# Optimization experiments

Hardware: AMD Instinct MI355X
Metric: run time of the kernel (lower is better)

## Reference

```python
import jax, jax.numpy as jnp
import numpy as np
import math

B, T, D, H = 4, 1024, 1024, 16
DK = D // H
TAU_THRESH = 0.3


def setup_inputs() -> dict:
    key = jax.random.key(0)
    ks = jax.random.split(key, 13)
    s = 1.0 / math.sqrt(D)
    return {
        "x": jax.random.normal(ks[0], (B, T, D), dtype=jnp.float32),
        "Wq": jax.random.normal(ks[1], (D, D), dtype=jnp.float32) * s,
        "bq": jax.random.normal(ks[2], (D,), dtype=jnp.float32) * s,
        "Wk": jax.random.normal(ks[3], (D, D), dtype=jnp.float32) * s,
        "bk": jax.random.normal(ks[4], (D,), dtype=jnp.float32) * s,
        "Wv": jax.random.normal(ks[5], (D, D), dtype=jnp.float32) * s,
        "bv": jax.random.normal(ks[6], (D,), dtype=jnp.float32) * s,
        "Wo": jax.random.normal(ks[7], (D, D), dtype=jnp.float32) * s,
        "bo": jax.random.normal(ks[8], (D,), dtype=jnp.float32) * s,
        "Wg1": jax.random.normal(ks[9], (1, D), dtype=jnp.float32) * s,
        "bg1": jax.random.normal(ks[10], (1,), dtype=jnp.float32) * s,
        "Wg2": jax.random.normal(ks[11], (1, D), dtype=jnp.float32) * s,
        "bg2": jax.random.normal(ks[12], (1,), dtype=jnp.float32) * s,
    }


def reference(x, Wq, bq, Wk, bk, Wv, bv, Wo, bo, Wg1, bg1, Wg2, bg2):
    b, t, d = x.shape
    # projections (torch Linear: y = x @ W.T + b)
    Q = (x @ Wq.T + bq).reshape(b, t, H, DK).transpose(0, 2, 1, 3)  # [B,H,T,dk]
    K = (x @ Wk.T + bk).reshape(b, t, H, DK).transpose(0, 2, 1, 3)
    V = (x @ Wv.T + bv).reshape(b, t, H, DK).transpose(0, 2, 1, 3)
    scores = jnp.einsum("bhqd,bhkd->bhqk", Q, K) / math.sqrt(DK)  # [B,H,T,T]
    # confidence gates from first-token query context [B, H*dk] = [B, D]
    context = Q[:, :, 0, :].reshape(b, d)
    q1 = jax.nn.sigmoid(context @ Wg1.T + bg1)  # [B,1]
    q2 = jax.nn.sigmoid(context @ Wg2.T + bg2)  # [B,1]
    c = jnp.clip(q1 * q2, 1e-8, 1.0)            # [B,1]
    tau = jnp.where(c < TAU_THRESH, 1.0 / c, jnp.ones_like(c)).reshape(b, 1, 1, 1)
    p = jax.nn.softmax(scores / tau, axis=-1)
    cb = c.reshape(b, 1, 1, 1)
    p_gated = cb * p + (1.0 - cb) * (1.0 / t)
    u = jnp.mean(1.0 - c, axis=-1, keepdims=True)  # [B,1]
    attn_out = jnp.einsum("bhqk,bhkd->bhqd", p_gated, V)
    attn_out = attn_out.transpose(0, 2, 1, 3).reshape(b, t, d)
    output = attn_out @ Wo.T + bo
    return output, u
```

## Files before the change

kernel.cpp:

```cpp
#include <hip/hip_runtime.h>
#include <stdint.h>

typedef short bf16x8 __attribute__((ext_vector_type(8)));
typedef float f32x4 __attribute__((ext_vector_type(4)));

#define MFMA_BF16(a, b, c) __builtin_amdgcn_mfma_f32_16x16x32_bf16((a), (b), (c), 0, 0, 0)

__device__ __forceinline__ short f2bf(float x) {
  union { float f; uint32_t u; } v; v.f = x;
  uint32_t r = (v.u + 0x7FFFu + ((v.u >> 16) & 1u)) >> 16;
  return (short)r;
}
__device__ __forceinline__ uint32_t rnd_bf_hi(float x) {
  union { float f; uint32_t u; } v; v.f = x;
  return v.u + 0x7FFFu + ((v.u >> 16) & 1u);
}
__device__ __forceinline__ uint32_t pack2bf(float a, float b) {
  return __builtin_amdgcn_perm(rnd_bf_hi(b), rnd_bf_hi(a), 0x07060302);
}
__device__ __forceinline__ float bfbits2f(uint32_t b16) {
  union { uint32_t u; float f; } v; v.u = b16 << 16; return v.f;
}
__device__ __forceinline__ float fexp2(float x) {
#if __has_builtin(__builtin_amdgcn_exp2f)
  return __builtin_amdgcn_exp2f(x);
#else
  return __expf(x * 0.6931471805599453f);
#endif
}
__device__ __forceinline__ void async16(const void* g, void* l) {
  __builtin_amdgcn_global_load_lds(
      (const __attribute__((address_space(1))) uint32_t*)g,
      (__attribute__((address_space(3))) uint32_t*)l, 16, 0, 0);
}

__global__ __launch_bounds__(256) void cvt_all(
    const float* __restrict__ x, const float* __restrict__ Wq,
    const float* __restrict__ Wk, const float* __restrict__ Wv,
    const float* __restrict__ Wo,
    short* __restrict__ xb, short* __restrict__ Wqb, short* __restrict__ Wkb,
    short* __restrict__ Wvb, short* __restrict__ Wob) {
  const int bid = blockIdx.x;
  const float* src; short* dst; int idx;
  if (bid < 4096) {
    src = x; dst = xb; idx = (bid << 8) + threadIdx.x;
  } else {
    const int r = bid - 4096;
    const int z = r >> 10;
    src = (z == 0) ? Wq : (z == 1) ? Wk : (z == 2) ? Wv : Wo;
    dst = (z == 0) ? Wqb : (z == 1) ? Wkb : (z == 2) ? Wvb : Wob;
    idx = ((r & 1023) << 8) + threadIdx.x;
  }
  float4 v = ((const float4*)src)[idx];
  short4 o;
  o.x = f2bf(v.x); o.y = f2bf(v.y); o.z = f2bf(v.z); o.w = f2bf(v.w);
  ((short4*)dst)[idx] = o;
}

__global__ __launch_bounds__(256) void gates_ctx(const float* __restrict__ x,
                                                 const float* __restrict__ Wq,
                                                 const float* __restrict__ bq,
                                                 float* __restrict__ ctx) {
  const int b = blockIdx.x;
  const int n0 = blockIdx.y << 6;
  __shared__ float xs[1024];
  const int tid = threadIdx.x;
  for (int i = tid; i < 1024; i += 256) xs[i] = x[b * 1048576 + i];
  __syncthreads();
  const int w = tid >> 6, lane = tid & 63;
  const float4* xv4 = (const float4*)xs;
  for (int rr = 0; rr < 16; ++rr) {
    const int n = n0 + (w << 4) + rr;
    const float4* wrow = (const float4*)(Wq + n * 1024);
    float p = 0.f;
#pragma unroll
    for (int c2 = 0; c2 < 4; ++c2) {
      float4 wv = wrow[lane + (c2 << 6)];
      float4 xv = xv4[lane + (c2 << 6)];
      p += xv.x * wv.x + xv.y * wv.y + xv.z * wv.z + xv.w * wv.w;
    }
#pragma unroll
    for (int off = 32; off; off >>= 1) p += __shfl_xor(p, off);
    if (lane == 0) ctx[b * 1024 + n] = p + bq[n];
  }
}

__global__ __launch_bounds__(256) void gates_fin(const float* __restrict__ ctx,
                                                 const float* __restrict__ Wg1,
                                                 const float* __restrict__ bg1,
                                                 const float* __restrict__ Wg2,
                                                 const float* __restrict__ bg2,
                                                 float* __restrict__ gates,
                                                 float* __restrict__ u_out) {
  __shared__ float red[16];
  const int tid = threadIdx.x, w = tid >> 6, lane = tid & 63;
  for (int b = 0; b < 4; ++b) {
    float4 cv = ((const float4*)(ctx + b * 1024))[tid];
    float4 w1 = ((const float4*)Wg1)[tid];
    float4 w2 = ((const float4*)Wg2)[tid];
    float p1 = cv.x * w1.x + cv.y * w1.y + cv.z * w1.z + cv.w * w1.w;
    float p2 = cv.x * w2.x + cv.y * w2.y + cv.z * w2.z + cv.w * w2.w;
#pragma unroll
    for (int off = 32; off; off >>= 1) { p1 += __shfl_xor(p1, off); p2 += __shfl_xor(p2, off); }
    if (lane == 0) { red[w] = p1; red[8 + w] = p2; }
    __syncthreads();
    if (tid == 0) {
      float g1 = red[0] + red[1] + red[2] + red[3] + bg1[0];
      float g2 = red[8] + red[9] + red[10] + red[11] + bg2[0];
      float q1 = 1.f / (1.f + expf(-g1));
      float q2 = 1.f / (1.f + expf(-g2));
      float c = fminf(fmaxf(q1 * q2, 1e-8f), 1.0f);
      gates[b * 2 + 0] = c;
      gates[b * 2 + 1] = (c < 0.3f ? c : 1.0f) * 0.125f;
      u_out[b] = 1.0f - c;
    }
    __syncthreads();
  }
}

__global__ __launch_bounds__(256) void gemm_qkv(
    const short* __restrict__ xb,
    const short* __restrict__ Wqb, const short* __restrict__ Wkb, const short* __restrict__ Wvb,
    const float* __restrict__ bq, const float* __restrict__ bk, const float* __restrict__ bv,
    const float* __restrict__ gat,
    short* __restrict__ Qh, short* __restrict__ Kh, short* __restrict__ Vt) {
  const int z = blockIdx.z;
  const short* W = (z == 0) ? Wqb : (z == 1) ? Wkb : Wvb;
  const float* bias = (z == 0) ? bq : (z == 1) ? bk : bv;

  const int m0 = blockIdx.x << 7;
  const int n0 = blockIdx.y << 7;
  const int tid = threadIdx.x;
  const int w = tid >> 6, lane = tid & 63;
  const int m15 = lane & 15, quad = lane >> 4;
  const int wr = w >> 1, wc = w & 1;

  const float qsc = (z == 0) ? gat[(m0 >> 10) * 2 + 1] * 1.4426950408889634f : 1.0f;

  __shared__ short As[4096];
  __shared__ short Bs[4096];
  __shared__ short Ts2[8192];

  f32x4 acc[4][4];
#pragma unroll
  for (int i = 0; i < 4; ++i)
#pragma unroll
    for (int j = 0; j < 4; ++j) { f32x4 zz = {0.f, 0.f, 0.f, 0.f}; acc[i][j] = zz; }

  const int srow = (w << 5) + (lane >> 2);
  const int scol = (lane & 3) << 3;
  const short* ga0 = xb + (m0 + srow) * 1024 + scol;
  const short* ga1 = ga0 + 16 * 1024;
  const short* gb0 = W + (n0 + srow) * 1024 + scol;
  const short* gb1 = gb0 + 16 * 1024;
  short* la0 = &As[srow * 32 + scol];
  short* la1 = la0 + 512;
  short* lb0 = &Bs[srow * 32 + scol];
  short* lb1 = lb0 + 512;

  for (int kt = 0; kt < 32; ++kt) {
    async16(ga0, la0); async16(ga1, la1);
    async16(gb0, lb0); async16(gb1, lb1);
    ga0 += 32; ga1 += 32; gb0 += 32; gb1 += 32;
    __syncthreads();
    bf16x8 a[4], b[4];
#pragma unroll
    for (int i = 0; i < 4; ++i)
      a[i] = *(const bf16x8*)(&As[((wr << 6) + (i << 4) + m15) * 32 + (quad << 3)]);
#pragma unroll
    for (int j = 0; j < 4; ++j)
      b[j] = *(const bf16x8*)(&Bs[((wc << 6) + (j << 4) + m15) * 32 + (quad << 3)]);
#pragma unroll
    for (int i = 0; i < 4; ++i)
#pragma unroll
      for (int j = 0; j < 4; ++j)
        acc[i][j] = MFMA_BF16(a[i], b[j], acc[i][j]);
    __syncthreads();
  }

  if (z == 2) {
    short* Ts = (w == 0) ? &As[0] : (w == 1) ? &Bs[0] : &Ts2[(w - 2) << 12];
    const int batch = m0 >> 10;
    const int tb0 = (m0 & 1023) + (wr << 6);
    const int h = (n0 >> 6) + wc;
#pragma unroll
    for (int j = 0; j < 4; ++j) {
      const int dkl = (j << 4) + m15;
      const float bb_ = bias[n0 + (wc << 6) + dkl];
#pragma unroll
      for (int i = 0; i < 4; ++i) {
        uint2 pk;
        pk.x = pack2bf(acc[i][j][0] + bb_, acc[i][j][1] + bb_);
        pk.y = pack2bf(acc[i][j][2] + bb_, acc[i][j][3] + bb_);
        const int blk = (i << 1) + (quad >> 1);
        const int addr = (dkl << 6) + ((blk ^ (dkl & 7)) << 3) + ((quad & 1) << 2);
        *(uint2*)&Ts[addr] = pk;
      }
    }
    __syncthreads();
    const int tb = lane & 7, dr = lane >> 3;
#pragma unroll
    for (int it = 0; it < 8; ++it) {
      const int dkl = dr + (it << 3);
      const int addr = (dkl << 6) + ((tb ^ (dkl & 7)) << 3);
      uint4 vv = *(const uint4*)&Ts[addr];
      *(uint4*)(Vt + ((((batch << 4) + h) << 6) + dkl) * 1024 + tb0 + (tb << 3)) = vv;
    }
  } else {
#pragma unroll
    for (int j = 0; j < 4; ++j) {
      const int n = n0 + (wc << 6) + (j << 4) + m15;
      const float bb_ = bias[n];
      const int h = n >> 6, dk = n & 63;
#pragma unroll
      for (int i = 0; i < 4; ++i) {
        const int mb = m0 + (wr << 6) + (i << 4) + (quad << 2);
#pragma unroll
        for (int r = 0; r < 4; ++r) {
          const int m = mb + r;
          const int batch = m >> 10, t = m & 1023;
          const short o = f2bf((acc[i][j][r] + bb_) * qsc);
          if (z == 1) Kh[((batch * 16 + h) * 1024 + t) * 64 + dk] = o;
          else        Qh[((batch * 16 + h) * 1024 + t) * 64 + dk] = o;
        }
      }
    }
  }
}

__global__ __launch_bounds__(256) void gemm_out(const short* __restrict__ Ab,
                                                const short* __restrict__ Wo,
                                                const float* __restrict__ bo,
                                                float* __restrict__ Cout) {
  const int m0 = blockIdx.x << 6;
  const int n0 = blockIdx.y << 7;
  const int tid = threadIdx.x;
  const int w = tid >> 6, lane = tid & 63;
  const int m15 = lane & 15, quad = lane >> 4;
  const int wr = w >> 1, wc = w & 1;

  __shared__ short As[2048];
  __shared__ short Bs[4096];

  f32x4 acc[2][4];
#pragma unroll
  for (int i = 0; i < 2; ++i)
#pragma unroll
    for (int j = 0; j < 4; ++j) { f32x4 zz = {0.f, 0.f, 0.f, 0.f}; acc[i][j] = zz; }

  const int arow = tid >> 2;
  const int acol = (tid & 3) << 3;
  const short* gA = Ab + (m0 + arow) * 1024 + acol;
  short* lA = &As[arow * 32 + acol];

  const int srow = (w << 5) + (lane >> 2);
  const int scol = (lane & 3) << 3;
  const short* gB0 = Wo + (n0 + srow) * 1024 + scol;
  const short* gB1 = gB0 + 16 * 1024;
  short* lB0 = &Bs[srow * 32 + scol];
  short* lB1 = lB0 + 512;

  for (int kt = 0; kt < 32; ++kt) {
    async16(gA, lA);
    async16(gB0, lB0); async16(gB1, lB1);
    gA += 32; gB0 += 32; gB1 += 32;
    __syncthreads();
    bf16x8 a[2], b[4];
#pragma unroll
    for (int i = 0; i < 2; ++i)
      a[i] = *(const bf16x8*)(&As[((wr << 5) + (i << 4) + m15) * 32 + (quad << 3)]);
#pragma unroll
    for (int j = 0; j < 4; ++j)
      b[j] = *(const bf16x8*)(&Bs[((wc << 6) + (j << 4) + m15) * 32 + (quad << 3)]);
#pragma unroll
    for (int i = 0; i < 2; ++i)
#pragma unroll
      for (int j = 0; j < 4; ++j)
        acc[i][j] = MFMA_BF16(a[i], b[j], acc[i][j]);
    __syncthreads();
  }

#pragma unroll
  for (int j = 0; j < 4; ++j) {
    const int n = n0 + (wc << 6) + (j << 4) + m15;
    const float bb_ = bo[n];
#pragma unroll
    for (int i = 0; i < 2; ++i) {
      const int mb = m0 + (wr << 5) + (i << 4) + (quad << 2);
#pragma unroll
      for (int r = 0; r < 4; ++r)
        Cout[(mb + r) * 1024 + n] = acc[i][j][r] + bb_;
    }
  }
}

__global__ __launch_bounds__(256) void meanv_k(const short* __restrict__ Vt,
                                               float* __restrict__ meanV) {
  const int bh = blockIdx.x;
  const int tid = threadIdx.x;
  const int d = tid >> 2, part = tid & 3;
  const short* row = Vt + bh * 65536 + d * 1024 + part * 256;
  float s = 0.f;
#pragma unroll 4
  for (int i = 0; i < 64; ++i) {
    uint2 v = *(const uint2*)(row + i * 4);
    s += bfbits2f(v.x & 0xffffu) + bfbits2f(v.x >> 16) +
         bfbits2f(v.y & 0xffffu) + bfbits2f(v.y >> 16);
  }
  s += __shfl_xor(s, 1);
  s += __shfl_xor(s, 2);
  if (part == 0) meanV[bh * 64 + d] = s * (1.0f / 1024.0f);
}

__global__ __launch_bounds__(256, 4) void attn_k(const short* __restrict__ Qh,
                                                 const short* __restrict__ Kh,
                                                 const short* __restrict__ Vt,
                                                 const float* __restrict__ gates,
                                                 const float* __restrict__ meanV,
                                                 short* __restrict__ attnb) {
  const int bh = blockIdx.x;
  const int b = bh >> 4, h = bh & 15;
  const int q0 = blockIdx.y << 6;
  const int tid = threadIdx.x;
  const int w = tid >> 6, lane = tid & 63;
  const int m15 = lane & 15, quad = lane >> 4;

  __shared__ short Ks[2][4096];
  __shared__ short Vs[2][4096];

  const short* ksrc = Kh + bh * 65536;
  const short* vsrc = Vt + bh * 65536;

  const short* qsrc = Qh + ((bh << 10) + q0 + (w << 4) + m15) * 64;
  const bf16x8 qb0 = *(const bf16x8*)(qsrc + (quad << 3));
  const bf16x8 qb1 = *(const bf16x8*)(qsrc + 32 + (quad << 3));

  const int off0 = tid, off1 = tid + 256;
  const int r0 = off0 >> 3, cb0 = (off0 & 7) ^ (r0 & 7);
  const int r1 = off1 >> 3, cb1 = (off1 & 7) ^ (r1 & 7);

#define STAGE(kv, bufi)                                                        \
  do {                                                                         \
    async16(ksrc + (((kv) << 6) + r0) * 64 + (cb0 << 3), &Ks[bufi][off0 << 3]);\
    async16(ksrc + (((kv) << 6) + r1) * 64 + (cb1 << 3), &Ks[bufi][off1 << 3]);\
    async16(vsrc + r0 * 1024 + ((kv) << 6) + (cb0 << 3), &Vs[bufi][off0 << 3]);\
    async16(vsrc + r1 * 1024 + ((kv) << 6) + (cb1 << 3), &Vs[bufi][off1 << 3]);\
  } while (0)

  STAGE(0, 0);

  float lsum = 0.f;
  f32x4 o_acc[4];
#pragma unroll
  for (int jd = 0; jd < 4; ++jd) { f32x4 zz = {0.f, 0.f, 0.f, 0.f}; o_acc[jd] = zz; }

  const int srcA = ((quad & 1) << 5) + m15;
  const int srcB = srcA + 16;
  const bool selhi = (quad & 2) != 0;

  for (int kv = 0; kv < 16; ++kv) {
    __syncthreads();
    if (kv < 15) STAGE(kv + 1, (kv + 1) & 1);
    const short* Kb = &Ks[kv & 1][0];
    const short* Vb = &Vs[kv & 1][0];

    f32x4 sacc[4];
#pragma unroll
    for (int s = 0; s < 4; ++s) {
      const int row = (s << 4) + m15;
      const int sw = row & 7;
      bf16x8 a0 = *(const bf16x8*)(Kb + (row << 6) + ((quad ^ sw) << 3));
      bf16x8 a1 = *(const bf16x8*)(Kb + (row << 6) + (((quad + 4) ^ sw) << 3));
      f32x4 zz = {0.f, 0.f, 0.f, 0.f};
      zz = MFMA_BF16(a0, qb0, zz);
      zz = MFMA_BF16(a1, qb1, zz);
      sacc[s] = zz;
    }

    uint32_t pk[4][2];
#pragma unroll
    for (int s = 0; s < 4; ++s) {
      float p0 = fexp2(sacc[s][0]);
      float p1 = fexp2(sacc[s][1]);
      float p2 = fexp2(sacc[s][2]);
      float p3 = fexp2(sacc[s][3]);
      lsum += (p0 + p1) + (p2 + p3);
      pk[s][0] = pack2bf(p0, p1);
      pk[s][1] = pack2bf(p2, p3);
    }

    bf16x8 pf[2];
#pragma unroll
    for (int H = 0; H < 2; ++H) {
      uint32_t f[4];
#pragma unroll
      for (int rp = 0; rp < 2; ++rp) {
        uint32_t alo = (uint32_t)__shfl((int)pk[2 * H][rp], srcA);
        uint32_t ahi = (uint32_t)__shfl((int)pk[2 * H + 1][rp], srcA);
        uint32_t blo = (uint32_t)__shfl((int)pk[2 * H][rp], srcB);
        uint32_t bhi = (uint32_t)__shfl((int)pk[2 * H + 1][rp], srcB);
        f[rp]     = selhi ? ahi : alo;
        f[2 + rp] = selhi ? bhi : blo;
      }
      pf[H] = *(bf16x8*)f;
    }

#pragma unroll
    for (int jd = 0; jd < 4; ++jd) {
      const int row = (jd << 4) + m15;
      const int sw = row & 7;
      bf16x8 v0 = *(const bf16x8*)(Vb + (row << 6) + ((quad ^ sw) << 3));
      bf16x8 v1 = *(const bf16x8*)(Vb + (row << 6) + (((quad + 4) ^ sw) << 3));
      o_acc[jd] = MFMA_BF16(v0, pf[0], o_acc[jd]);
      o_acc[jd] = MFMA_BF16(v1, pf[1], o_acc[jd]);
    }
  }
#undef STAGE

  float l = lsum;
  l += __shfl_xor(l, 16);
  l += __shfl_xor(l, 32);

  const float cg = gates[b * 2 + 0];
  const float s0 = cg / l;
  const float omc = 1.0f - cg;
  const int qrow = q0 + (w << 4) + m15;
  short* orow = attnb + ((b << 10) + qrow) * 1024 + (h << 6);
#pragma unroll
  for (int jd = 0; jd < 4; ++jd) {
    float4 mv = *(const float4*)(meanV + (bh << 6) + (jd << 4) + (quad << 2));
    float v0_ = s0 * o_acc[jd][0] + omc * mv.x;
    float v1_ = s0 * o_acc[jd][1] + omc * mv.y;
    float v2_ = s0 * o_acc[jd][2] + omc * mv.z;
    float v3_ = s0 * o_acc[jd][3] + omc * mv.w;
    uint2 st;
    st.x = pack2bf(v0_, v1_);
    st.y = pack2bf(v2_, v3_);
    *(uint2*)(orow + (jd << 4) + (quad << 2)) = st;
  }
}

extern "C" void kernel_launch(void* const* d_in, const int* in_sizes, int n_in,
                              void* d_out, int out_size, void* d_ws, size_t ws_size,
                              hipStream_t stream) {
  const float* x   = (const float*)d_in[0];
  const float* Wq  = (const float*)d_in[1];
  const float* bq  = (const float*)d_in[2];
  const float* Wk  = (const float*)d_in[3];
  const float* bk  = (const float*)d_in[4];
  const float* Wv  = (const float*)d_in[5];
  const float* bv  = (const float*)d_in[6];
  const float* Wo  = (const float*)d_in[7];
  const float* bo  = (const float*)d_in[8];
  const float* Wg1 = (const float*)d_in[9];
  const float* bg1 = (const float*)d_in[10];
  const float* Wg2 = (const float*)d_in[11];
  const float* bg2 = (const float*)d_in[12];
  float* out = (float*)d_out;

  char* ws = (char*)d_ws;
  short* xb   = (short*)(ws + 0);
  short* Wqb  = (short*)(ws + 8388608);
  short* Wkb  = (short*)(ws + 10485760);
  short* Wvb  = (short*)(ws + 12582912);
  short* Wob  = (short*)(ws + 14680064);
  short* Qh   = (short*)(ws + 16777216);
  short* Kh   = (short*)(ws + 25165824);
  short* Vt   = (short*)(ws + 33554432);
  short* attb = (short*)(ws + 41943040);
  float* ctx  = (float*)(ws + 50331648);
  float* gat  = (float*)(ws + 50348032);
  float* mV   = (float*)(ws + 50348064);

  cvt_all<<<8192, 256, 0, stream>>>(x, Wq, Wk, Wv, Wo, xb, Wqb, Wkb, Wvb, Wob);

  gates_ctx<<<dim3(4, 16), 256, 0, stream>>>(x, Wq, bq, ctx);
  gates_fin<<<1, 256, 0, stream>>>(ctx, Wg1, bg1, Wg2, bg2, gat, out + 4194304);

  gemm_qkv<<<dim3(32, 8, 3), 256, 0, stream>>>(xb, Wqb, Wkb, Wvb, bq, bk, bv, gat, Qh, Kh, Vt);
  meanv_k<<<64, 256, 0, stream>>>(Vt, mV);
  attn_k<<<dim3(64, 16), 256, 0, stream>>>(Qh, Kh, Vt, gat, mV, attb);
  gemm_out<<<dim3(64, 8), 256, 0, stream>>>(attb, Wob, bo, out);
}
```

Measured before the change: 222.3 us.

## Swizzle GEMM LDS tiles, fuse gate-context into conversion kernel, drop V transpose staging

Merges the fp32-to-bf16 conversion and gate-context matvec into one launch, removing a kernel launch. Both GEMMs now load LDS tiles with an XOR swizzle on the 16-byte column block, aimed at avoiding bank conflicts on the MFMA operand reads. The V projection epilogue no longer stages through shared memory for the transpose. It writes 8-byte packed chunks straight to the transposed Vt layout, which saves LDS space and a barrier but makes the global stores narrower and less coalesced.

```diff
diff --git a/kernel.cpp b/kernel.cpp
--- a/kernel.cpp
+++ b/kernel.cpp
@@ -34,54 +34,52 @@
       (__attribute__((address_space(3))) uint32_t*)l, 16, 0, 0);
 }
 
-__global__ __launch_bounds__(256) void cvt_all(
+__global__ __launch_bounds__(256) void prep_k(
     const float* __restrict__ x, const float* __restrict__ Wq,
     const float* __restrict__ Wk, const float* __restrict__ Wv,
-    const float* __restrict__ Wo,
+    const float* __restrict__ Wo, const float* __restrict__ bq,
     short* __restrict__ xb, short* __restrict__ Wqb, short* __restrict__ Wkb,
-    short* __restrict__ Wvb, short* __restrict__ Wob) {
+    short* __restrict__ Wvb, short* __restrict__ Wob, float* __restrict__ ctx) {
+  __shared__ float xs[1024];
   const int bid = blockIdx.x;
-  const float* src; short* dst; int idx;
-  if (bid < 4096) {
-    src = x; dst = xb; idx = (bid << 8) + threadIdx.x;
+  const int tid = threadIdx.x;
+  if (bid < 8192) {
+    const float* src; short* dst; int idx;
+    if (bid < 4096) {
+      src = x; dst = xb; idx = (bid << 8) + tid;
+    } else {
+      const int r = bid - 4096;
+      const int z = r >> 10;
+      src = (z == 0) ? Wq : (z == 1) ? Wk : (z == 2) ? Wv : Wo;
+      dst = (z == 0) ? Wqb : (z == 1) ? Wkb : (z == 2) ? Wvb : Wob;
+      idx = ((r & 1023) << 8) + tid;
+    }
+    float4 v = ((const float4*)src)[idx];
+    short4 o;
+    o.x = f2bf(v.x); o.y = f2bf(v.y); o.z = f2bf(v.z); o.w = f2bf(v.w);
+    ((short4*)dst)[idx] = o;
   } else {
-    const int r = bid - 4096;
-    const int z = r >> 10;
-    src = (z == 0) ? Wq : (z == 1) ? Wk : (z == 2) ? Wv : Wo;
-    dst = (z == 0) ? Wqb : (z == 1) ? Wkb : (z == 2) ? Wvb : Wob;
-    idx = ((r & 1023) << 8) + threadIdx.x;
-  }
-  float4 v = ((const float4*)src)[idx];
-  short4 o;
-  o.x = f2bf(v.x); o.y = f2bf(v.y); o.z = f2bf(v.z); o.w = f2bf(v.w);
-  ((short4*)dst)[idx] = o;
-}
-
-__global__ __launch_bounds__(256) void gates_ctx(const float* __restrict__ x,
-                                                 const float* __restrict__ Wq,
-                                                 const float* __restrict__ bq,
-                                                 float* __restrict__ ctx) {
-  const int b = blockIdx.x;
-  const int n0 = blockIdx.y << 6;
-  __shared__ float xs[1024];
-  const int tid = threadIdx.x;
-  for (int i = tid; i < 1024; i += 256) xs[i] = x[b * 1048576 + i];
-  __syncthreads();
-  const int w = tid >> 6, lane = tid & 63;
-  const float4* xv4 = (const float4*)xs;
-  for (int rr = 0; rr < 16; ++rr) {
-    const int n = n0 + (w << 4) + rr;
-    const float4* wrow = (const float4*)(Wq + n * 1024);
-    float p = 0.f;
-#pragma unroll
-    for (int c2 = 0; c2 < 4; ++c2) {
-      float4 wv = wrow[lane + (c2 << 6)];
-      float4 xv = xv4[lane + (c2 << 6)];
-      p += xv.x * wv.x + xv.y * wv.y + xv.z * wv.z + xv.w * wv.w;
-    }
-#pragma unroll
-    for (int off = 32; off; off >>= 1) p += __shfl_xor(p, off);
-    if (lane == 0) ctx[b * 1024 + n] = p + bq[n];
+    const int r = bid - 8192;
+    const int b = r >> 4;
+    const int n0 = (r & 15) << 6;
+    for (int i = tid; i < 1024; i += 256) xs[i] = x[b * 1048576 + i];
+    __syncthreads();
+    const int w = tid >> 6, lane = tid & 63;
+    const float4* xv4 = (const float4*)xs;
+    for (int rr = 0; rr < 16; ++rr) {
+      const int n = n0 + (w << 4) + rr;
+      const float4* wrow = (const float4*)(Wq + n * 1024);
+      float p = 0.f;
+#pragma unroll
+      for (int c2 = 0; c2 < 4; ++c2) {
+        float4 wv = wrow[lane + (c2 << 6)];
+        float4 xv = xv4[lane + (c2 << 6)];
+        p += xv.x * wv.x + xv.y * wv.y + xv.z * wv.z + xv.w * wv.w;
+      }
+#pragma unroll
+      for (int off = 32; off; off >>= 1) p += __shfl_xor(p, off);
+      if (lane == 0) ctx[b * 1024 + n] = p + bq[n];
+    }
   }
 }
 
@@ -139,7 +137,6 @@
 
   __shared__ short As[4096];
   __shared__ short Bs[4096];
-  __shared__ short Ts2[8192];
 
   f32x4 acc[4][4];
 #pragma unroll
@@ -147,16 +144,17 @@
 #pragma unroll
     for (int j = 0; j < 4; ++j) { f32x4 zz = {0.f, 0.f, 0.f, 0.f}; acc[i][j] = zz; }
 
-  const int srow = (w << 5) + (lane >> 2);
-  const int scol = (lane & 3) << 3;
-  const short* ga0 = xb + (m0 + srow) * 1024 + scol;
-  const short* ga1 = ga0 + 16 * 1024;
-  const short* gb0 = W + (n0 + srow) * 1024 + scol;
-  const short* gb1 = gb0 + 16 * 1024;
-  short* la0 = &As[srow * 32 + scol];
-  short* la1 = la0 + 512;
-  short* lb0 = &Bs[srow * 32 + scol];
-  short* lb1 = lb0 + 512;
+  const int s0 = tid, s1 = tid + 256;
+  const int row0 = s0 >> 2, lcb0 = (s0 & 3) ^ ((row0 >> 1) & 3);
+  const int row1 = s1 >> 2, lcb1 = (s1 & 3) ^ ((row1 >> 1) & 3);
+  const short* ga0 = xb + (m0 + row0) * 1024 + (lcb0 << 3);
+  const short* ga1 = xb + (m0 + row1) * 1024 + (lcb1 << 3);
+  const short* gb0 = W + (n0 + row0) * 1024 + (lcb0 << 3);
+  const short* gb1 = W + (n0 + row1) * 1024 + (lcb1 << 3);
+  short* la0 = &As[s0 << 3];
+  short* la1 = &As[s1 << 3];
+  short* lb0 = &Bs[s0 << 3];
+  short* lb1 = &Bs[s1 << 3];
 
   for (int kt = 0; kt < 32; ++kt) {
     async16(ga0, la0); async16(ga1, la1);
@@ -165,11 +163,15 @@
     __syncthreads();
     bf16x8 a[4], b[4];
 #pragma unroll
-    for (int i = 0; i < 4; ++i)
-      a[i] = *(const bf16x8*)(&As[((wr << 6) + (i << 4) + m15) * 32 + (quad << 3)]);
-#pragma unroll
-    for (int j = 0; j < 4; ++j)
-      b[j] = *(const bf16x8*)(&Bs[((wc << 6) + (j << 4) + m15) * 32 + (quad << 3)]);
+    for (int i = 0; i < 4; ++i) {
+      const int ra = (wr << 6) + (i << 4) + m15;
+      a[i] = *(const bf16x8*)(&As[ra * 32 + ((quad ^ ((ra >> 1) & 3)) << 3)]);
+    }
+#pragma unroll
+    for (int j = 0; j < 4; ++j) {
+      const int rb = (wc << 6) + (j << 4) + m15;
+      b[j] = *(const bf16x8*)(&Bs[rb * 32 + ((quad ^ ((rb >> 1) & 3)) << 3)]);
+    }
 #pragma unroll
     for (int i = 0; i < 4; ++i)
 #pragma unroll
@@ -179,32 +181,21 @@
   }
 
   if (z == 2) {
-    short* Ts = (w == 0) ? &As[0] : (w == 1) ? &Bs[0] : &Ts2[(w - 2) << 12];
     const int batch = m0 >> 10;
-    const int tb0 = (m0 & 1023) + (wr << 6);
-    const int h = (n0 >> 6) + wc;
 #pragma unroll
     for (int j = 0; j < 4; ++j) {
-      const int dkl = (j << 4) + m15;
-      const float bb_ = bias[n0 + (wc << 6) + dkl];
+      const int n = n0 + (wc << 6) + (j << 4) + m15;
+      const float bb_ = bias[n];
+      const int h = n >> 6, dk = n & 63;
+      short* vrow = Vt + ((((batch << 4) + h) << 6) + dk) * 1024;
 #pragma unroll
       for (int i = 0; i < 4; ++i) {
+        const int t = (m0 & 1023) + (wr << 6) + (i << 4) + (quad << 2);
         uint2 pk;
         pk.x = pack2bf(acc[i][j][0] + bb_, acc[i][j][1] + bb_);
         pk.y = pack2bf(acc[i][j][2] + bb_, acc[i][j][3] + bb_);
-        const int blk = (i << 1) + (quad >> 1);
-        const int addr = (dkl << 6) + ((blk ^ (dkl & 7)) << 3) + ((quad & 1) << 2);
-        *(uint2*)&Ts[addr] = pk;
+        *(uint2*)(vrow + t) = pk;
       }
-    }
-    __syncthreads();
-    const int tb = lane & 7, dr = lane >> 3;
-#pragma unroll
-    for (int it = 0; it < 8; ++it) {
-      const int dkl = dr + (it << 3);
-      const int addr = (dkl << 6) + ((tb ^ (dkl & 7)) << 3);
-      uint4 vv = *(const uint4*)&Ts[addr];
-      *(uint4*)(Vt + ((((batch << 4) + h) << 6) + dkl) * 1024 + tb0 + (tb << 3)) = vv;
     }
   } else {
 #pragma unroll
@@ -248,17 +239,16 @@
 #pragma unroll
     for (int j = 0; j < 4; ++j) { f32x4 zz = {0.f, 0.f, 0.f, 0.f}; acc[i][j] = zz; }
 
-  const int arow = tid >> 2;
-  const int acol = (tid & 3) << 3;
-  const short* gA = Ab + (m0 + arow) * 1024 + acol;
-  short* lA = &As[arow * 32 + acol];
-
-  const int srow = (w << 5) + (lane >> 2);
-  const int scol = (lane & 3) << 3;
-  const short* gB0 = Wo + (n0 + srow) * 1024 + scol;
-  const short* gB1 = gB0 + 16 * 1024;
-  short* lB0 = &Bs[srow * 32 + scol];
-  short* lB1 = lB0 + 512;
+  const int s0 = tid, s1 = tid + 256;
+  const int arow = s0 >> 2, alcb = (s0 & 3) ^ ((arow >> 1) & 3);
+  const int brow0 = s0 >> 2, blcb0 = alcb;
+  const int brow1 = s1 >> 2, blcb1 = (s1 & 3) ^ ((brow1 >> 1) & 3);
+  const short* gA  = Ab + (m0 + arow) * 1024 + (alcb << 3);
+  const short* gB0 = Wo + (n0 + brow0) * 1024 + (blcb0 << 3);
+  const short* gB1 = Wo + (n0 + brow1) * 1024 + (blcb1 << 3);
+  short* lA  = &As[s0 << 3];
+  short* lB0 = &Bs[s0 << 3];
+  short* lB1 = &Bs[s1 << 3];
 
   for (int kt = 0; kt < 32; ++kt) {
     async16(gA, lA);
@@ -267,11 +257,15 @@
     __syncthreads();
     bf16x8 a[2], b[4];
 #pragma unroll
-    for (int i = 0; i < 2; ++i)
-      a[i] = *(const bf16x8*)(&As[((wr << 5) + (i << 4) + m15) * 32 + (quad << 3)]);
-#pragma unroll
-    for (int j = 0; j < 4; ++j)
-      b[j] = *(const bf16x8*)(&Bs[((wc << 6) + (j << 4) + m15) * 32 + (quad << 3)]);
+    for (int i = 0; i < 2; ++i) {
+      const int ra = (wr << 5) + (i << 4) + m15;
+      a[i] = *(const bf16x8*)(&As[ra * 32 + ((quad ^ ((ra >> 1) & 3)) << 3)]);
+    }
+#pragma unroll
+    for (int j = 0; j < 4; ++j) {
+      const int rb = (wc << 6) + (j << 4) + m15;
+      b[j] = *(const bf16x8*)(&Bs[rb * 32 + ((quad ^ ((rb >> 1) & 3)) << 3)]);
+    }
 #pragma unroll
     for (int i = 0; i < 2; ++i)
 #pragma unroll
@@ -472,9 +466,8 @@
   float* gat  = (float*)(ws + 50348032);
   float* mV   = (float*)(ws + 50348064);
 
-  cvt_all<<<8192, 256, 0, stream>>>(x, Wq, Wk, Wv, Wo, xb, Wqb, Wkb, Wvb, Wob);
-
-  gates_ctx<<<dim3(4, 16), 256, 0, stream>>>(x, Wq, bq, ctx);
+  prep_k<<<8256, 256, 0, stream>>>(x, Wq, Wk, Wv, Wo, bq,
+                                   xb, Wqb, Wkb, Wvb, Wob, ctx);
   gates_fin<<<1, 256, 0, stream>>>(ctx, Wg1, bg1, Wg2, bg2, gat, out + 4194304);
 
   gemm_qkv<<<dim3(32, 8, 3), 256, 0, stream>>>(xb, Wqb, Wkb, Wvb, bq, bk, bv, gat, Qh, Kh, Vt);
```

New measurement: 218.6 us. Within noise of the previous version (-1.7%).
